# Kernel tuning notes

Measured on AMD Instinct MI355X. Metric: run time of the kernel, lower is better.

The kernel has to match this reference:

```python
import jax, jax.numpy as jnp
import numpy as np

N_MAX = 5000  # original module truncates both clouds to 5000 points


def _hungarian(cost):
    """Exact linear sum assignment (Jonker-Volgenant / Hungarian with potentials).
    cost: (n, n) float64 numpy array. Returns cols: cols[i] = column assigned to row i.
    Matches scipy.optimize.linear_sum_assignment on square matrices."""
    n = cost.shape[0]
    u = np.zeros(n + 1)
    v = np.zeros(n + 1)
    p = np.full(n + 1, -1, dtype=np.int64)  # p[j] = row matched to column j (-1 = free); col n is virtual
    way = np.zeros(n, dtype=np.int64)
    for i in range(n):
        p[n] = i
        j0 = n
        minv = np.full(n, np.inf)
        used = np.zeros(n + 1, dtype=bool)
        # Dijkstra-style shortest augmenting path, inner step vectorized over columns
        while p[j0] != -1:
            used[j0] = True
            i0 = p[j0]
            free = ~used[:n]
            cur = cost[i0] - u[i0] - v[:n]
            upd = free & (cur < minv)
            minv = np.where(upd, cur, minv)
            way = np.where(upd, j0, way)
            masked = np.where(free, minv, np.inf)
            j1 = int(np.argmin(masked))
            delta = masked[j1]
            used_idx = np.nonzero(used)[0]
            u[p[used_idx]] += delta
            v[used_idx] -= delta
            minv = np.where(free, minv - delta, minv)
            j0 = j1
        # augment along alternating path back to the virtual column
        while j0 != n:
            j1 = way[j0]
            p[j0] = p[j1]
            j0 = int(j1)
    cols = np.empty(n, dtype=np.int64)
    cols[p[:n]] = np.arange(n)
    return cols


def _pairwise_dist(a, b):
    # Euclidean cdist: (n,3) x (m,3) -> (n,m)
    d2 = (jnp.sum(a * a, axis=1)[:, None]
          + jnp.sum(b * b, axis=1)[None, :]
          - 2.0 * (a @ b.T))
    return jnp.sqrt(jnp.maximum(d2, 0.0))


def setup_inputs() -> dict:
    key = jax.random.key(0)
    k1, k2 = jax.random.split(key)
    gt_pc = jax.random.normal(k1, (1, 1024, 3), dtype=jnp.float32)
    gen_pc = jax.random.normal(k2, (1, 1024, 3), dtype=jnp.float32)
    return {"gt_pc": gt_pc, "gen_pc": gen_pc}


def reference(gt_pc, gen_pc):
    # squeeze() + truncate to 5000 points, as in the torch module
    a = gt_pc.reshape(-1, gt_pc.shape[-1])[:N_MAX]
    b = gen_pc.reshape(-1, gen_pc.shape[-1])[:N_MAX]
    d = _pairwise_dist(a, b)  # (n, n) full cost matrix
    # exact optimal assignment (host-side, data dependent -> not jittable)
    cols = _hungarian(np.asarray(d, dtype=np.float64))
    rows = jnp.arange(d.shape[0])
    return d[rows, jnp.asarray(cols)].mean()
```

## Files before the change

kernel.cpp:

```cpp
#include <hip/hip_runtime.h>
#include <math.h>


#define N        1024
#define NT       512
#define NW       (NT / 64)
#define CPL      16
#define NPHASE   5
#define ROUND_CAP 40000

typedef unsigned long long ull;

__device__ __forceinline__ float wave_min_bcast(float x) {
#define DPPSTEP(C) { int _t = __builtin_amdgcn_update_dpp(                    \
      __float_as_int(x), __float_as_int(x), (C), 0xf, 0xf, false);            \
      x = fminf(x, __int_as_float(_t)); }
    DPPSTEP(0x111)
    DPPSTEP(0x112)
    DPPSTEP(0x114)
    DPPSTEP(0x118)
    DPPSTEP(0x142)
    DPPSTEP(0x143)
#undef DPPSTEP
    return __int_as_float(__builtin_amdgcn_readlane(__float_as_int(x), 63));
}

__device__ __forceinline__ float dist_b(const float4 Ai, float bxn, float byn,
                                        float bzn, float sbk) {
    float acc = fmaf(bzn, Ai.z, sbk);
    acc = fmaf(byn, Ai.y, acc);
    acc = fmaf(bxn, Ai.x, acc);
    return __builtin_amdgcn_sqrtf(fmaxf(acc + Ai.w, 0.0f));
}

__global__ __launch_bounds__(NT, 1)
void emd_auction(const float* __restrict__ gt, const float* __restrict__ gen,
                 float* __restrict__ out)
{
    __shared__ float4 A[N];
    __shared__ float4 B[N];
    __shared__ float  p[N];
    __shared__ ull    bidPack[N];
    __shared__ int    owner[N];
    __shared__ int    pobj[N];
    __shared__ int    freeL[N];
    __shared__ int    s_nfree;
    __shared__ double partial[NW];

    const int tid  = threadIdx.x;
    const int lane = tid & 63;
    const int wid  = tid >> 6;

    float bxn[CPL], byn[CPL], bzn[CPL], sb[CPL];
    #pragma unroll
    for (int k = 0; k < CPL; ++k) {
        const int j = (k << 6) | lane;
        const float gx = gen[3*j], gy = gen[3*j+1], gz = gen[3*j+2];
        bxn[k] = -2.f*gx; byn[k] = -2.f*gy; bzn[k] = -2.f*gz;
        sb[k]  = gx*gx + gy*gy + gz*gz;
    }
    for (int i = tid; i < N; i += NT) {
        const float x = gt[3*i], y = gt[3*i+1], z = gt[3*i+2];
        A[i] = make_float4(x, y, z, x*x + y*y + z*z);
        const float gx = gen[3*i], gy = gen[3*i+1], gz = gen[3*i+2];
        B[i] = make_float4(gx, gy, gz, gx*gx + gy*gy + gz*gz);
        p[i] = 0.f;
        bidPack[i] = 0ull;
    }
    __syncthreads();

    const float EPS[NPHASE] = {0.4f, 0.07f, 0.012f, 2.5e-3f, 5e-4f};
    int rounds = 0;

    for (int ph = 0; ph < NPHASE; ++ph) {
        const float eps = EPS[ph];
        for (int i = tid; i < N; i += NT) {
            owner[i] = -1; pobj[i] = -1; freeL[i] = i;
        }
        if (tid == 0) s_nfree = N;
        __syncthreads();

        for (;;) {
            const int nf = s_nfree;
            if (nf == 0 || rounds >= ROUND_CAP) break;
            ++rounds;

            for (int t = wid; t < nf; t += NW) {
                const int i = freeL[t];
                const float4 Ai = A[i];
                float m1 = INFINITY, m2 = INFINITY; int a1 = 0;
                #pragma unroll
                for (int k = 0; k < CPL; ++k) {
                    const int j = (k << 6) | lane;
                    const float rc = dist_b(Ai, bxn[k], byn[k], bzn[k], sb[k])
                                   + p[j];
                    if (rc < m1)      { m2 = m1; m1 = rc; a1 = j; }
                    else if (rc < m2) { m2 = rc; }
                }
                const float g1 = wave_min_bcast(m1);
                const ull  mm  = __ballot(m1 == g1);
                const int  w1  = __ffsll(mm) - 1;
                const int  j1  = __builtin_amdgcn_readlane(a1, w1);
                const float contrib = (lane == w1) ? m2 : m1;
                const float g2 = wave_min_bcast(contrib);
                const float bid = p[j1] + (g2 - g1) + eps;
                if (lane == 0)
                    atomicMax(&bidPack[j1],
                              ((ull)(unsigned)__float_as_int(bid) << 32)
                              | (unsigned)i);
            }
            __syncthreads();

            if (tid == 0) s_nfree = 0;
            for (int j = tid; j < N; j += NT) {
                const ull pk = bidPack[j];
                if (pk) {
                    bidPack[j] = 0ull;
                    p[j] = __int_as_float((int)(pk >> 32));
                    const int inew = (int)(pk & 0xffffffffu);
                    const int iold = owner[j];
                    owner[j] = inew;
                    pobj[inew] = j;
                    if (iold >= 0) pobj[iold] = -1;
                }
            }
            __syncthreads();

            for (int base = 0; base < N; base += NT) {
                const int i = base + tid;
                const bool fr = (pobj[i] < 0);
                const ull m = __ballot(fr);
                int pos = 0;
                if (lane == 0 && m) pos = atomicAdd(&s_nfree, __popcll(m));
                pos = __shfl(pos, 0);
                if (fr) freeL[pos + __popcll(m & ((1ull << lane) - 1ull))] = i;
            }
            __syncthreads();
        }
    }

    if (s_nfree > 0) {
        const int nf = s_nfree;
        if (wid == 0) {
            for (int t = 0; t < nf; ++t) {
                const int i = freeL[t];
                const float4 Ai = A[i];
                float m1 = INFINITY; int a1 = 0;
                #pragma unroll
                for (int k = 0; k < CPL; ++k) {
                    const int j = (k << 6) | lane;
                    const bool fre = (owner[j] < 0);
                    const float c = dist_b(Ai, bxn[k], byn[k], bzn[k], sb[k]);
                    const float sel = fre ? c : INFINITY;
                    if (sel < m1) { m1 = sel; a1 = j; }
                }
                const float g1 = wave_min_bcast(m1);
                const ull  mm  = __ballot(m1 == g1);
                const int  w1  = __ffsll(mm) - 1;
                const int  j1  = __builtin_amdgcn_readlane(a1, w1);
                if (lane == 0) owner[j1] = i;
            }
        }
        __syncthreads();
    }

    double s = 0.0;
    for (int j = tid; j < N; j += NT) {
        const int i = owner[j];
        if (i >= 0) {
            const float4 Ai = A[i];
            const float4 Bj = B[j];
            const float dot = Ai.x*Bj.x + Ai.y*Bj.y + Ai.z*Bj.z;
            const float d2  = Ai.w + Bj.w - 2.0f*dot;
            s += (double)__builtin_amdgcn_sqrtf(fmaxf(d2, 0.0f));
        }
    }
    #pragma unroll
    for (int m = 32; m >= 1; m >>= 1) s += __shfl_xor(s, m);
    if (lane == 0) partial[wid] = s;
    __syncthreads();
    if (tid == 0) {
        double tot = 0.0;
        for (int w = 0; w < NW; ++w) tot += partial[w];
        out[0] = (float)(tot / (double)N);
    }
}

extern "C" void kernel_launch(void* const* d_in, const int* in_sizes, int n_in,
                              void* d_out, int out_size, void* d_ws, size_t ws_size,
                              hipStream_t stream) {
    const float* gt  = (const float*)d_in[0];
    const float* gen = (const float*)d_in[1];
    float* out = (float*)d_out;
    emd_auction<<<1, NT, 0, stream>>>(gt, gen, out);
}
```

Measured before the change: 9.696 ms.

## Add single-wave Gauss-Seidel auction tail and sparse bid/free-list bookkeeping

Doubles the block to 1024 threads. When few bidders remain, one wave switches to sequential Gauss-Seidel bidding, which removes the block-wide barrier rounds that dominate the long tail of the auction. The Jacobi rounds now track only the objects that received bids and rebuild the next free list from the current free list instead of scanning all N entries each round. This adds atomics and a double-buffered free list, and the round cap is lowered, which could change the assignment in edge cases.

```diff
diff --git a/kernel.cpp b/kernel.cpp
--- a/kernel.cpp
+++ b/kernel.cpp
@@ -2,12 +2,14 @@
 #include <math.h>
 
 
-#define N        1024
-#define NT       512
-#define NW       (NT / 64)
-#define CPL      16
-#define NPHASE   5
-#define ROUND_CAP 40000
+#define N         1024
+#define NT        1024
+#define NW        (NT / 64)
+#define CPL       16
+#define NPHASE    5
+#define GS_T      64
+#define GS_BUDGET 60000
+#define ROUND_CAP 20000
 
 typedef unsigned long long ull;
 
@@ -43,8 +45,12 @@
     __shared__ ull    bidPack[N];
     __shared__ int    owner[N];
     __shared__ int    pobj[N];
-    __shared__ int    freeL[N];
-    __shared__ int    s_nfree;
+    __shared__ int    freeBuf[2][N];
+    __shared__ int    bidList[N];
+    __shared__ int    bidFlag[N];
+    __shared__ int    s_cnt[2];
+    __shared__ int    s_nbid;
+    __shared__ int    s_fail;
     __shared__ double partial[NW];
 
     const int tid  = threadIdx.x;
@@ -64,36 +70,90 @@
         A[i] = make_float4(x, y, z, x*x + y*y + z*z);
         const float gx = gen[3*i], gy = gen[3*i+1], gz = gen[3*i+2];
         B[i] = make_float4(gx, gy, gz, gx*gx + gy*gy + gz*gz);
-        p[i] = 0.f;
-        bidPack[i] = 0ull;
-    }
+        p[i] = 0.f; bidPack[i] = 0ull; bidFlag[i] = 0;
+    }
+    if (tid == 0) { s_fail = 0; s_nbid = 0; }
     __syncthreads();
 
     const float EPS[NPHASE] = {0.4f, 0.07f, 0.012f, 2.5e-3f, 5e-4f};
-    int rounds = 0;
-
-    for (int ph = 0; ph < NPHASE; ++ph) {
+    int  rounds  = 0;
+    bool aborted = false;
+    int  cur     = 0;
+
+    for (int ph = 0; ph < NPHASE && !aborted; ++ph) {
         const float eps = EPS[ph];
         for (int i = tid; i < N; i += NT) {
-            owner[i] = -1; pobj[i] = -1; freeL[i] = i;
-        }
-        if (tid == 0) s_nfree = N;
+            owner[i] = -1; pobj[i] = -1; freeBuf[0][i] = i;
+        }
+        if (tid == 0) { s_cnt[0] = N; s_cnt[1] = 0; }
+        cur = 0;
         __syncthreads();
 
         for (;;) {
-            const int nf = s_nfree;
-            if (nf == 0 || rounds >= ROUND_CAP) break;
-            ++rounds;
+            const int nf = s_cnt[cur];
+            const int fl = s_fail;
+            if (nf == 0 || fl) break;
+            if (++rounds >= ROUND_CAP) { aborted = true; break; }
+
+            if (nf <= GS_T) {
+                if (wid == 0) {
+                    int n2 = nf, bids = 0;
+                    while (n2 > 0 && bids < GS_BUDGET) {
+                        ++bids;
+                        const int i = freeBuf[cur][n2 - 1];
+                        const float4 Ai = A[i];
+                        float m1 = INFINITY, m2 = INFINITY; int a1 = 0;
+                        #pragma unroll
+                        for (int k = 0; k < CPL; ++k) {
+                            const int j = (k << 6) | lane;
+                            const float rc =
+                                dist_b(Ai, bxn[k], byn[k], bzn[k], sb[k]) + p[j];
+                            if (rc < m1)      { m2 = m1; m1 = rc; a1 = j; }
+                            else if (rc < m2) { m2 = rc; }
+                        }
+                        const float g1 = wave_min_bcast(m1);
+                        const ull  mm  = __ballot(m1 == g1);
+                        const int  w1  = __ffsll(mm) - 1;
+                        const int  j1  = __builtin_amdgcn_readlane(a1, w1);
+                        const float contrib = (lane == w1) ? m2 : m1;
+                        const float g2 = wave_min_bcast(contrib);
+                        const float pj1  = p[j1];
+                        const int   iold = owner[j1];
+                        if (lane == 0) {
+                            p[j1] = pj1 + (g2 - g1) + eps;
+                            owner[j1] = i; pobj[i] = j1;
+                        }
+                        if (iold >= 0) {
+                            if (lane == 0) {
+                                pobj[iold] = -1;
+                                freeBuf[cur][n2 - 1] = iold;
+                            }
+                        } else {
+                            --n2;
+                        }
+                        asm volatile("s_waitcnt lgkmcnt(0)" ::: "memory");
+                    }
+                    if (lane == 0) {
+                        s_cnt[cur] = n2;
+                        if (n2 > 0) s_fail = 1;
+                    }
+                }
+                __syncthreads();
+                continue;
+            }
+
+            const int nxt = cur ^ 1;
+            if (tid == 0) s_cnt[nxt] = 0;
 
             for (int t = wid; t < nf; t += NW) {
-                const int i = freeL[t];
+                const int i = freeBuf[cur][t];
                 const float4 Ai = A[i];
                 float m1 = INFINITY, m2 = INFINITY; int a1 = 0;
                 #pragma unroll
                 for (int k = 0; k < CPL; ++k) {
                     const int j = (k << 6) | lane;
-                    const float rc = dist_b(Ai, bxn[k], byn[k], bzn[k], sb[k])
-                                   + p[j];
+                    const float rc =
+                        dist_b(Ai, bxn[k], byn[k], bzn[k], sb[k]) + p[j];
                     if (rc < m1)      { m2 = m1; m1 = rc; a1 = j; }
                     else if (rc < m2) { m2 = rc; }
                 }
@@ -103,65 +163,81 @@
                 const int  j1  = __builtin_amdgcn_readlane(a1, w1);
                 const float contrib = (lane == w1) ? m2 : m1;
                 const float g2 = wave_min_bcast(contrib);
-                const float bid = p[j1] + (g2 - g1) + eps;
-                if (lane == 0)
+                if (lane == 0) {
+                    const float bid = p[j1] + (g2 - g1) + eps;
                     atomicMax(&bidPack[j1],
                               ((ull)(unsigned)__float_as_int(bid) << 32)
                               | (unsigned)i);
-            }
-            __syncthreads();
-
-            if (tid == 0) s_nfree = 0;
-            for (int j = tid; j < N; j += NT) {
+                    if (atomicCAS(&bidFlag[j1], 0, 1) == 0) {
+                        const int pos = atomicAdd(&s_nbid, 1);
+                        bidList[pos] = j1;
+                    }
+                }
+            }
+            __syncthreads();
+
+            const int nbid = s_nbid;
+            for (int t = tid; t < nbid; t += NT) {
+                const int j  = bidList[t];
                 const ull pk = bidPack[j];
-                if (pk) {
-                    bidPack[j] = 0ull;
-                    p[j] = __int_as_float((int)(pk >> 32));
-                    const int inew = (int)(pk & 0xffffffffu);
-                    const int iold = owner[j];
-                    owner[j] = inew;
-                    pobj[inew] = j;
-                    if (iold >= 0) pobj[iold] = -1;
-                }
-            }
-            __syncthreads();
-
-            for (int base = 0; base < N; base += NT) {
-                const int i = base + tid;
-                const bool fr = (pobj[i] < 0);
+                bidPack[j] = 0ull; bidFlag[j] = 0;
+                p[j] = __int_as_float((int)(pk >> 32));
+                const int inew = (int)(pk & 0xffffffffu);
+                const int iold = owner[j];
+                owner[j] = inew;
+                pobj[inew] = j;
+                if (iold >= 0) {
+                    pobj[iold] = -1;
+                    const int pos = atomicAdd(&s_cnt[nxt], 1);
+                    freeBuf[nxt][pos] = iold;
+                }
+            }
+            __syncthreads();
+
+            if (tid == 0) s_nbid = 0;
+            for (int base = 0; base < nf; base += NT) {
+                const int t = base + tid;
+                bool fr = false; int i = 0;
+                if (t < nf) { i = freeBuf[cur][t]; fr = (pobj[i] < 0); }
                 const ull m = __ballot(fr);
                 int pos = 0;
-                if (lane == 0 && m) pos = atomicAdd(&s_nfree, __popcll(m));
+                if (lane == 0 && m) pos = atomicAdd(&s_cnt[nxt], __popcll(m));
                 pos = __shfl(pos, 0);
-                if (fr) freeL[pos + __popcll(m & ((1ull << lane) - 1ull))] = i;
-            }
-            __syncthreads();
-        }
-    }
-
-    if (s_nfree > 0) {
-        const int nf = s_nfree;
-        if (wid == 0) {
-            for (int t = 0; t < nf; ++t) {
-                const int i = freeL[t];
-                const float4 Ai = A[i];
-                float m1 = INFINITY; int a1 = 0;
-                #pragma unroll
-                for (int k = 0; k < CPL; ++k) {
-                    const int j = (k << 6) | lane;
-                    const bool fre = (owner[j] < 0);
-                    const float c = dist_b(Ai, bxn[k], byn[k], bzn[k], sb[k]);
-                    const float sel = fre ? c : INFINITY;
-                    if (sel < m1) { m1 = sel; a1 = j; }
-                }
-                const float g1 = wave_min_bcast(m1);
-                const ull  mm  = __ballot(m1 == g1);
-                const int  w1  = __ffsll(mm) - 1;
-                const int  j1  = __builtin_amdgcn_readlane(a1, w1);
-                if (lane == 0) owner[j1] = i;
-            }
-        }
-        __syncthreads();
+                if (fr)
+                    freeBuf[nxt][pos + __popcll(m & ((1ull << lane) - 1ull))] = i;
+            }
+            __syncthreads();
+            cur = nxt;
+        }
+        if (s_fail) aborted = true;
+    }
+
+    {
+        const int leftover = s_cnt[cur];
+        if (leftover > 0) {
+            if (wid == 0) {
+                for (int t = 0; t < leftover; ++t) {
+                    const int i = freeBuf[cur][t];
+                    const float4 Ai = A[i];
+                    float m1 = INFINITY; int a1 = 0;
+                    #pragma unroll
+                    for (int k = 0; k < CPL; ++k) {
+                        const int j = (k << 6) | lane;
+                        const bool fre = (owner[j] < 0);
+                        const float c = dist_b(Ai, bxn[k], byn[k], bzn[k], sb[k]);
+                        const float sel = fre ? c : INFINITY;
+                        if (sel < m1) { m1 = sel; a1 = j; }
+                    }
+                    const float g1 = wave_min_bcast(m1);
+                    const ull  mm  = __ballot(m1 == g1);
+                    const int  w1  = __ffsll(mm) - 1;
+                    const int  j1  = __builtin_amdgcn_readlane(a1, w1);
+                    if (lane == 0) owner[j1] = i;
+                    asm volatile("s_waitcnt lgkmcnt(0)" ::: "memory");
+                }
+            }
+            __syncthreads();
+        }
     }
 
     double s = 0.0;
```

After: 22.09 ms. +127.9%, slower.

## Replace synchronous auction rounds with asynchronous Gauss-Seidel wave bidding and warm-start phases

Applied to the files above, without the earlier changes.

The kernel replaces the Jacobi-style auction, which needs three block barriers per round, with an asynchronous scheme. Each wave pulls a free person from a shared stack and bids with a single atomicMax on a packed (price, owner) word, then carries on bidding for whoever it evicted. Epsilon-scaling drops to three phases and keeps the assignments that stay eps-complementary-slack between phases instead of resetting them all. The block doubles to 1024 threads. Lock-free updates and volatile price reads bring in races, and the larger final epsilon could change accuracy. A per-wave bid cap falls back to greedy completion if it is hit.

```diff
diff --git a/kernel.cpp b/kernel.cpp
--- a/kernel.cpp
+++ b/kernel.cpp
@@ -2,14 +2,15 @@
 #include <math.h>
 
 
-#define N        1024
-#define NT       512
-#define NW       (NT / 64)
-#define CPL      16
-#define NPHASE   5
-#define ROUND_CAP 40000
+#define N       1024
+#define NT      1024
+#define NW      (NT / 64)
+#define CPL     16
+#define NPHASE  3
+#define WAVE_BID_CAP 60000
 
 typedef unsigned long long ull;
+#define NOOWN 0xFFFFFFFFu
 
 __device__ __forceinline__ float wave_min_bcast(float x) {
 #define DPPSTEP(C) { int _t = __builtin_amdgcn_update_dpp(                    \
@@ -39,17 +40,18 @@
 {
     __shared__ float4 A[N];
     __shared__ float4 B[N];
-    __shared__ float  p[N];
-    __shared__ ull    bidPack[N];
-    __shared__ int    owner[N];
-    __shared__ int    pobj[N];
-    __shared__ int    freeL[N];
-    __shared__ int    s_nfree;
+    __shared__ ull    pack[N];
+    __shared__ int    stk[N];
+    __shared__ unsigned char matched[N];
+    __shared__ int    s_head, s_scount, s_nfree, s_fail;
     __shared__ double partial[NW];
 
     const int tid  = threadIdx.x;
     const int lane = tid & 63;
     const int wid  = tid >> 6;
+    volatile int* vnfree = &s_nfree;
+    volatile int* vfail  = &s_fail;
+    volatile unsigned* vpack = (volatile unsigned*)pack;
 
     float bxn[CPL], byn[CPL], bzn[CPL], sb[CPL];
     #pragma unroll
@@ -64,101 +66,140 @@
         A[i] = make_float4(x, y, z, x*x + y*y + z*z);
         const float gx = gen[3*i], gy = gen[3*i+1], gz = gen[3*i+2];
         B[i] = make_float4(gx, gy, gz, gx*gx + gy*gy + gz*gz);
-        p[i] = 0.f;
-        bidPack[i] = 0ull;
-    }
+        pack[i] = (ull)NOOWN;
+        matched[i] = 0;
+    }
+    if (tid == 0) s_fail = 0;
     __syncthreads();
 
-    const float EPS[NPHASE] = {0.4f, 0.07f, 0.012f, 2.5e-3f, 5e-4f};
-    int rounds = 0;
+    const float EPS[NPHASE] = {0.25f, 0.033f, 4e-3f};
 
     for (int ph = 0; ph < NPHASE; ++ph) {
+        if (s_fail) break;
         const float eps = EPS[ph];
-        for (int i = tid; i < N; i += NT) {
-            owner[i] = -1; pobj[i] = -1; freeL[i] = i;
-        }
-        if (tid == 0) s_nfree = N;
-        __syncthreads();
-
-        for (;;) {
-            const int nf = s_nfree;
-            if (nf == 0 || rounds >= ROUND_CAP) break;
-            ++rounds;
-
-            for (int t = wid; t < nf; t += NW) {
-                const int i = freeL[t];
-                const float4 Ai = A[i];
-                float m1 = INFINITY, m2 = INFINITY; int a1 = 0;
+
+        if (ph > 0) {
+            for (int i = tid; i < N; i += NT) matched[i] = 0;
+            __syncthreads();
+            for (int j = wid; j < N; j += NW) {
+                const unsigned ow = (unsigned)(pack[j] & 0xffffffffu);
+                if (ow == NOOWN) continue;
+                const float4 Ai = A[ow];
+                float m1 = INFINITY;
                 #pragma unroll
                 for (int k = 0; k < CPL; ++k) {
-                    const int j = (k << 6) | lane;
-                    const float rc = dist_b(Ai, bxn[k], byn[k], bzn[k], sb[k])
-                                   + p[j];
-                    if (rc < m1)      { m2 = m1; m1 = rc; a1 = j; }
-                    else if (rc < m2) { m2 = rc; }
+                    const int jj = (k << 6) | lane;
+                    const float pj = __int_as_float(vpack[(jj << 1) | 1]);
+                    m1 = fminf(m1, dist_b(Ai, bxn[k], byn[k], bzn[k], sb[k]) + pj);
                 }
                 const float g1 = wave_min_bcast(m1);
-                const ull  mm  = __ballot(m1 == g1);
-                const int  w1  = __ffsll(mm) - 1;
-                const int  j1  = __builtin_amdgcn_readlane(a1, w1);
-                const float contrib = (lane == w1) ? m2 : m1;
-                const float g2 = wave_min_bcast(contrib);
-                const float bid = p[j1] + (g2 - g1) + eps;
-                if (lane == 0)
-                    atomicMax(&bidPack[j1],
-                              ((ull)(unsigned)__float_as_int(bid) << 32)
-                              | (unsigned)i);
+                if (lane == 0) {
+                    const float4 Bj = B[j];
+                    const float dot = Ai.x*Bj.x + Ai.y*Bj.y + Ai.z*Bj.z;
+                    const float rcj = __builtin_amdgcn_sqrtf(
+                        fmaxf(Ai.w + Bj.w - 2.f*dot, 0.f))
+                        + __int_as_float(vpack[(j << 1) | 1]);
+                    if (rcj > g1 + eps)
+                        pack[j] = (pack[j] & 0xffffffff00000000ull) | NOOWN;
+                    else
+                        matched[ow] = 1;
+                }
             }
             __syncthreads();
-
-            if (tid == 0) s_nfree = 0;
-            for (int j = tid; j < N; j += NT) {
-                const ull pk = bidPack[j];
-                if (pk) {
-                    bidPack[j] = 0ull;
-                    p[j] = __int_as_float((int)(pk >> 32));
-                    const int inew = (int)(pk & 0xffffffffu);
-                    const int iold = owner[j];
-                    owner[j] = inew;
-                    pobj[inew] = j;
-                    if (iold >= 0) pobj[iold] = -1;
-                }
-            }
-            __syncthreads();
-
-            for (int base = 0; base < N; base += NT) {
-                const int i = base + tid;
-                const bool fr = (pobj[i] < 0);
-                const ull m = __ballot(fr);
-                int pos = 0;
-                if (lane == 0 && m) pos = atomicAdd(&s_nfree, __popcll(m));
-                pos = __shfl(pos, 0);
-                if (fr) freeL[pos + __popcll(m & ((1ull << lane) - 1ull))] = i;
-            }
-            __syncthreads();
-        }
-    }
-
-    if (s_nfree > 0) {
-        const int nf = s_nfree;
+        }
+
+        if (tid == 0) { s_scount = 0; s_head = 0; }
+        __syncthreads();
+        {
+            const int i = tid;
+            const bool fr = (matched[i] == 0);
+            const ull m = __ballot(fr);
+            int pos = 0;
+            if (lane == 0 && m) pos = atomicAdd(&s_scount, __popcll(m));
+            pos = __shfl(pos, 0);
+            if (fr) stk[pos + __popcll(m & ((1ull << lane) - 1ull))] = i;
+        }
+        __syncthreads();
+        if (tid == 0) s_nfree = s_scount;
+        __syncthreads();
+
+        int person = -1, mybids = 0;
+        for (;;) {
+            if (*vfail) break;
+            if (person < 0) {
+                int idx = 0;
+                if (lane == 0) idx = atomicAdd(&s_head, 1);
+                idx = __shfl(idx, 0);
+                if (idx < s_scount) person = stk[idx];
+                else {
+                    if (*vnfree == 0) break;
+                    __builtin_amdgcn_s_sleep(2);
+                    continue;
+                }
+            }
+            const float4 Ai = A[person];
+            float m1 = INFINITY, m2 = INFINITY, c1 = 0.f; int a1 = 0;
+            #pragma unroll
+            for (int k = 0; k < CPL; ++k) {
+                const int jj = (k << 6) | lane;
+                const float pj = __int_as_float(vpack[(jj << 1) | 1]);
+                const float c  = dist_b(Ai, bxn[k], byn[k], bzn[k], sb[k]);
+                const float rc = c + pj;
+                if (rc < m1)      { m2 = m1; m1 = rc; a1 = jj; c1 = c; }
+                else if (rc < m2) { m2 = rc; }
+            }
+            const float g1 = wave_min_bcast(m1);
+            const ull  bm  = __ballot(m1 == g1);
+            const int  w1  = __ffsll(bm) - 1;
+            const float contrib = (lane == w1) ? m2 : m1;
+            const float g2 = wave_min_bcast(contrib);
+            int winl = 0, evict = 0;
+            if (lane == w1) {
+                const float bid = (g2 - c1) + eps;
+                const ull np = ((ull)(unsigned)__float_as_int(bid) << 32)
+                             | (unsigned)person;
+                const ull old = atomicMax(&pack[a1], np);
+                winl  = (old < np) ? 1 : 0;
+                evict = (int)(old & 0xffffffffu);
+                if (winl && evict < 0) atomicSub(&s_nfree, 1);
+            }
+            winl  = __shfl(winl,  w1);
+            evict = __shfl(evict, w1);
+            if (winl) person = evict;
+            if (++mybids > WAVE_BID_CAP) { if (lane == 0) s_fail = 1; break; }
+        }
+        __syncthreads();
+    }
+
+    if (s_fail) {
+        for (int i = tid; i < N; i += NT) matched[i] = 0;
+        __syncthreads();
+        for (int j = tid; j < N; j += NT) {
+            const unsigned ow = (unsigned)(pack[j] & 0xffffffffu);
+            if (ow != NOOWN) matched[ow] = 1;
+        }
+        __syncthreads();
         if (wid == 0) {
-            for (int t = 0; t < nf; ++t) {
-                const int i = freeL[t];
+            for (int i = 0; i < N; ++i) {
+                if (matched[i]) continue;
                 const float4 Ai = A[i];
                 float m1 = INFINITY; int a1 = 0;
                 #pragma unroll
                 for (int k = 0; k < CPL; ++k) {
-                    const int j = (k << 6) | lane;
-                    const bool fre = (owner[j] < 0);
+                    const int jj = (k << 6) | lane;
+                    const bool fre =
+                        ((unsigned)(pack[jj] & 0xffffffffu) == NOOWN);
                     const float c = dist_b(Ai, bxn[k], byn[k], bzn[k], sb[k]);
                     const float sel = fre ? c : INFINITY;
-                    if (sel < m1) { m1 = sel; a1 = j; }
+                    if (sel < m1) { m1 = sel; a1 = jj; }
                 }
                 const float g1 = wave_min_bcast(m1);
-                const ull  mm  = __ballot(m1 == g1);
-                const int  w1  = __ffsll(mm) - 1;
+                const ull  bm  = __ballot(m1 == g1);
+                const int  w1  = __ffsll(bm) - 1;
                 const int  j1  = __builtin_amdgcn_readlane(a1, w1);
-                if (lane == 0) owner[j1] = i;
+                if (lane == 0)
+                    pack[j1] = (pack[j1] & 0xffffffff00000000ull) | (unsigned)i;
+                asm volatile("s_waitcnt lgkmcnt(0)" ::: "memory");
             }
         }
         __syncthreads();
@@ -166,9 +207,9 @@
 
     double s = 0.0;
     for (int j = tid; j < N; j += NT) {
-        const int i = owner[j];
-        if (i >= 0) {
-            const float4 Ai = A[i];
+        const unsigned ow = (unsigned)(pack[j] & 0xffffffffu);
+        if (ow != NOOWN) {
+            const float4 Ai = A[ow];
             const float4 Bj = B[j];
             const float dot = Ai.x*Bj.x + Ai.y*Bj.y + Ai.z*Bj.z;
             const float d2  = Ai.w + Bj.w - 2.0f*dot;
```

Result: slower. 11.54 ms (+19.0%).
